# Kernel tuning notes

Measured on AMD Instinct MI355X. Metric: run time of the kernel, lower is better.

Reference implementation:

```python
import jax, jax.numpy as jnp
import numpy as np

B, L, D = 4, 2048, 1024
H = 16
HD = D // H


def setup_inputs() -> dict:
    key = jax.random.key(0)
    ks = jax.random.split(key, 6)
    x = jax.random.normal(ks[0], (B, L, D), dtype=jnp.float32)
    # True = masked-out (strict upper triangle -> causal)
    causal_mask = jnp.triu(jnp.ones((L, L), dtype=bool), k=1)
    key_padding_mask = jnp.zeros((B, L), dtype=bool)  # no padding
    lim = 1.0 / np.sqrt(D)
    Wqkv = jax.random.uniform(ks[1], (3 * D, D), minval=-lim, maxval=lim, dtype=jnp.float32)
    bqkv = jax.random.uniform(ks[2], (3 * D,), minval=-lim, maxval=lim, dtype=jnp.float32)
    Wproj = jax.random.uniform(ks[3], (D, D), minval=-lim, maxval=lim, dtype=jnp.float32)
    bproj = jax.random.uniform(ks[4], (D,), minval=-lim, maxval=lim, dtype=jnp.float32)
    return {"x": x, "causal_mask": causal_mask, "key_padding_mask": key_padding_mask,
            "Wqkv": Wqkv, "bqkv": bqkv, "Wproj": Wproj, "bproj": bproj}


def reference(x, causal_mask, key_padding_mask, Wqkv, bqkv, Wproj, bproj):
    b, l, d = x.shape
    scale = (d // H // 1) ** 0  # placeholder; real scale below
    scale = (d // H) ** -0.5
    qkv = x @ Wqkv.T + bqkv                      # [B,L,3D]
    qkv = qkv.reshape(b, l, 3, H, HD).transpose(2, 0, 3, 1, 4)  # [3,B,H,L,HD]
    q, k, v = qkv[0], qkv[1], qkv[2]
    attn = jnp.einsum('bhqd,bhkd->bhqk', q, k) * scale          # [B,H,L,L]
    neg_inf = jnp.float32(-jnp.inf)
    attn = jnp.where(causal_mask[None, None, :, :], neg_inf, attn)
    attn = jnp.where(key_padding_mask[:, None, None, :], neg_inf, attn)
    attn = jax.nn.softmax(attn, axis=-1)
    attn = jnp.nan_to_num(attn, nan=0.0, posinf=0.0, neginf=0.0)
    out = jnp.einsum('bhqk,bhkd->bhqd', attn, v)                # [B,H,L,HD]
    out = out.transpose(0, 2, 1, 3).reshape(b, l, d)
    return out @ Wproj.T + bproj
```

## Files before the change

### kernel.cpp

```cpp
#include <hip/hip_runtime.h>

typedef __bf16 bf16;
typedef __attribute__((ext_vector_type(8))) __bf16 bf16x8;
typedef __attribute__((ext_vector_type(4))) __bf16 bf16x4;
typedef __attribute__((ext_vector_type(4))) float f32x4;
typedef __attribute__((ext_vector_type(4))) short short4v;

#define AS1C(p) ((const __attribute__((address_space(1))) void*)(p))
#define AS3(p)  ((__attribute__((address_space(3))) void*)(p))

static __device__ __forceinline__ f32x4 pv_mfma(bf16x4 a, bf16x4 b, f32x4 c) {
#if __has_builtin(__builtin_amdgcn_mfma_f32_16x16x16bf16_1k)
  return __builtin_amdgcn_mfma_f32_16x16x16bf16_1k(
      __builtin_bit_cast(short4v, a), __builtin_bit_cast(short4v, b), c, 0, 0, 0);
#else
  f32x4 d = c;
  asm("v_mfma_f32_16x16x16_bf16 %0, %1, %2, %0" : "+v"(d) : "v"(a), "v"(b));
  return d;
#endif
}

__global__ void castk(const float* __restrict__ in, bf16* __restrict__ out, long n) {
  long i = ((long)blockIdx.x * blockDim.x + threadIdx.x) * 4;
  if (i >= n) return;
  f32x4 v = *reinterpret_cast<const f32x4*>(in + i);
  bf16x4 o;
  o[0] = (bf16)v[0]; o[1] = (bf16)v[1]; o[2] = (bf16)v[2]; o[3] = (bf16)v[3];
  *reinterpret_cast<bf16x4*>(out + i) = o;
}

template<int MODE>
__global__ __launch_bounds__(256, 2)
void gemm_bt(const bf16* __restrict__ A, const bf16* __restrict__ BT,
             const float* __restrict__ bias, void* __restrict__ Cout,
             int M, int N, int K) {
  __shared__ bf16 As[128 * 64];
  __shared__ bf16 Bs[128 * 64];
  const int tid = threadIdx.x;
  const int lane = tid & 63;
  const int w = tid >> 6;
  const int wm = w >> 1, wn = w & 1;
  const int row0 = blockIdx.y * 128, col0 = blockIdx.x * 128;

  f32x4 acc[4][4] = {};

  const int srow = tid >> 3;
  const int scb = ((tid & 7) << 4) ^ ((srow & 7) << 4);
  const long aoff = (long)(row0 + srow) * K + (scb >> 1);
  const long boff = (long)(col0 + srow) * K + (scb >> 1);

  for (int k0 = 0; k0 < K; k0 += 64) {
    #pragma unroll
    for (int i = 0; i < 4; ++i) {
      __builtin_amdgcn_global_load_lds(AS1C(A + aoff + (long)i * 32 * K + k0),
                                       AS3((char*)As + i * 4096 + w * 1024), 16, 0, 0);
      __builtin_amdgcn_global_load_lds(AS1C(BT + boff + (long)i * 32 * K + k0),
                                       AS3((char*)Bs + i * 4096 + w * 1024), 16, 0, 0);
    }
    __syncthreads();
    #pragma unroll
    for (int kf = 0; kf < 2; ++kf) {
      bf16x8 af[4], bfr[4];
      #pragma unroll
      for (int m = 0; m < 4; ++m) {
        int r = wm * 64 + m * 16 + (lane & 15);
        int cb = (kf * 64 + ((lane >> 4) << 4)) ^ ((r & 7) << 4);
        af[m] = *reinterpret_cast<const bf16x8*>((const char*)As + r * 128 + cb);
      }
      #pragma unroll
      for (int n = 0; n < 4; ++n) {
        int r = wn * 64 + n * 16 + (lane & 15);
        int cb = (kf * 64 + ((lane >> 4) << 4)) ^ ((r & 7) << 4);
        bfr[n] = *reinterpret_cast<const bf16x8*>((const char*)Bs + r * 128 + cb);
      }
      #pragma unroll
      for (int m = 0; m < 4; ++m)
        #pragma unroll
        for (int n = 0; n < 4; ++n) {
          if constexpr (MODE == 1)
            acc[m][n] = __builtin_amdgcn_mfma_f32_16x16x32_bf16(bfr[n], af[m], acc[m][n], 0, 0, 0);
          else
            acc[m][n] = __builtin_amdgcn_mfma_f32_16x16x32_bf16(af[m], bfr[n], acc[m][n], 0, 0, 0);
        }
    }
    __syncthreads();
  }

  const int g = lane >> 4, q = lane & 15;

  if constexpr (MODE == 0) {
    #pragma unroll
    for (int m = 0; m < 4; ++m)
      #pragma unroll
      for (int n = 0; n < 4; ++n)
        #pragma unroll
        for (int r = 0; r < 4; ++r) {
          int grow = row0 + wm * 64 + m * 16 + g * 4 + r;
          int gcol = col0 + wn * 64 + n * 16 + q;
          reinterpret_cast<float*>(Cout)[(long)grow * N + gcol] = acc[m][n][r] + bias[gcol];
        }
  } else if constexpr (MODE == 1) {
    const int t = (int)blockIdx.x >> 3;
    const int h = (((int)blockIdx.x << 1) | wn) & 15;
    const float qs = (t == 0) ? 0.125f : 1.0f;
    bf16* outb = reinterpret_cast<bf16*>(Cout) + (t ? 8388608 : 0);
    #pragma unroll
    for (int n = 0; n < 4; ++n) {
      f32x4 bv = *reinterpret_cast<const f32x4*>(bias + col0 + wn * 64 + n * 16 + g * 4);
      #pragma unroll
      for (int m = 0; m < 4; ++m) {
        int grow = row0 + wm * 64 + m * 16 + q;
        int bb = grow >> 11, ll = grow & 2047;
        bf16x4 o;
        #pragma unroll
        for (int r = 0; r < 4; ++r) o[r] = (bf16)((acc[m][n][r] + bv[r]) * qs);
        *reinterpret_cast<bf16x4*>(outb + ((long)(bb * 16 + h) * 2048 + ll) * 64 + n * 16 + g * 4) = o;
      }
    }
  } else {
    const int h = (((int)blockIdx.x << 1) | wn) & 15;
    bf16* outb = reinterpret_cast<bf16*>(Cout);
    #pragma unroll
    for (int n = 0; n < 4; ++n) {
      float bv = bias[col0 + wn * 64 + n * 16 + q];
      int hd = n * 16 + q;
      #pragma unroll
      for (int m = 0; m < 4; ++m) {
        int grow = row0 + wm * 64 + m * 16 + g * 4;
        int bb = grow >> 11, ll = grow & 2047;
        bf16x4 o;
        #pragma unroll
        for (int r = 0; r < 4; ++r) o[r] = (bf16)(acc[m][n][r] + bv);
        *reinterpret_cast<bf16x4*>(outb + ((long)(bb * 16 + h) * 64 + hd) * 2048 + ll) = o;
      }
    }
  }
}

__global__ __launch_bounds__(256, 4)
void attn_fwd(const bf16* __restrict__ Qg, const bf16* __restrict__ Kg,
              const bf16* __restrict__ VTg, bf16* __restrict__ Og) {
  __shared__ bf16 Ks[2][64 * 64];
  __shared__ bf16 Vs[2][64 * 64];
  const int tid = threadIdx.x, lane = tid & 63, w = tid >> 6;
  const int g = lane >> 4, q = lane & 15;

  const int orig = blockIdx.x;
  const int wgid = (orig & 7) * 256 + (orig >> 3);
  const int bh = wgid >> 5;
  const int qi = 31 - (wgid & 31);
  const int bb = bh >> 4, h = bh & 15;
  const long base = (long)bh * (2048 * 64);
  const int qw = qi * 64 + w * 16;
  const int myq = qw + q;

  bf16x8 qf[2];
  qf[0] = *reinterpret_cast<const bf16x8*>(Qg + base + (long)myq * 64 + g * 8);
  qf[1] = *reinterpret_cast<const bf16x8*>(Qg + base + (long)myq * 64 + 32 + g * 8);

  f32x4 accO[4] = {};
  float m = -1e30f, l = 0.f;

  const int srow = tid >> 3;
  const int scb = ((tid & 7) << 4) ^ ((srow & 7) << 4);
  const int nt = qi + 1;

  auto stage = [&](int kt, int buf) {
    #pragma unroll
    for (int i = 0; i < 2; ++i) {
      __builtin_amdgcn_global_load_lds(
          AS1C(Kg + base + (long)(kt * 64 + i * 32 + srow) * 64 + (scb >> 1)),
          AS3((char*)&Ks[buf][0] + i * 4096 + w * 1024), 16, 0, 0);
      __builtin_amdgcn_global_load_lds(
          AS1C(VTg + base + (long)(i * 32 + srow) * 2048 + kt * 64 + (scb >> 1)),
          AS3((char*)&Vs[buf][0] + i * 4096 + w * 1024), 16, 0, 0);
    }
  };

  stage(0, 0);

  for (int kt = 0; kt < nt; ++kt) {
    const int cur = kt & 1;
    __syncthreads();
    if (kt + 1 < nt) stage(kt + 1, cur ^ 1);

    const char* Kb = (const char*)&Ks[cur][0];
    const char* Vb = (const char*)&Vs[cur][0];

    f32x4 sT[4] = {};
    #pragma unroll
    for (int kf = 0; kf < 2; ++kf) {
      #pragma unroll
      for (int a = 0; a < 4; ++a) {
        int r = a * 16 + q;
        int cb = (kf * 64 + g * 16) ^ ((r & 7) << 4);
        bf16x8 kb = *reinterpret_cast<const bf16x8*>(Kb + r * 128 + cb);
        sT[a] = __builtin_amdgcn_mfma_f32_16x16x32_bf16(kb, qf[kf], sT[a], 0, 0, 0);
      }
    }

    if (kt == qi) {
      #pragma unroll
      for (int a = 0; a < 4; ++a)
        #pragma unroll
        for (int r = 0; r < 4; ++r) {
          int kv = kt * 64 + a * 16 + 4 * g + r;
          if (kv > myq) sT[a][r] = -1e30f;
        }
    }

    float vm = -1e30f;
    #pragma unroll
    for (int a = 0; a < 4; ++a)
      #pragma unroll
      for (int r = 0; r < 4; ++r) vm = fmaxf(vm, sT[a][r]);
    vm = fmaxf(vm, __shfl_xor(vm, 16));
    vm = fmaxf(vm, __shfl_xor(vm, 32));
    float mnew = fmaxf(m, vm);
    float fac = __expf(m - mnew);
    m = mnew;

    float ps = 0.f;
    bf16x4 pa[4];
    #pragma unroll
    for (int a = 0; a < 4; ++a)
      #pragma unroll
      for (int r = 0; r < 4; ++r) {
        float p = __expf(sT[a][r] - mnew);
        ps += p;
        pa[a][r] = (bf16)p;
      }
    ps += __shfl_xor(ps, 16);
    ps += __shfl_xor(ps, 32);
    l = l * fac + ps;
    #pragma unroll
    for (int b = 0; b < 4; ++b) accO[b] *= fac;

    #pragma unroll
    for (int a = 0; a < 4; ++a) {
      #pragma unroll
      for (int b = 0; b < 4; ++b) {
        int row = b * 16 + q;
        int cb = (a * 32 + g * 8) ^ ((row & 7) << 4);
        bf16x4 vfrag = *reinterpret_cast<const bf16x4*>(Vb + row * 128 + cb);
        accO[b] = pv_mfma(vfrag, pa[a], accO[b]);
      }
    }
  }

  __syncthreads();
  char* ob = (char*)&Ks[0][0] + w * 2048;
  float rl = 1.0f / l;
  #pragma unroll
  for (int b = 0; b < 4; ++b)
    #pragma unroll
    for (int r = 0; r < 4; ++r) {
      int hd = 16 * b + 4 * g + r;
      int cb = (hd * 2) ^ ((q & 7) << 4);
      *reinterpret_cast<bf16*>(ob + q * 128 + cb) = (bf16)(accO[b][r] * rl);
    }
  asm volatile("s_waitcnt lgkmcnt(0)" ::: "memory");
  __builtin_amdgcn_sched_barrier(0);

  const int rr = lane >> 2, cc = lane & 3;
  #pragma unroll
  for (int half = 0; half < 2; ++half) {
    int hd0 = cc * 16 + half * 8;
    int cb = (hd0 * 2) ^ ((rr & 7) << 4);
    bf16x8 vv = *reinterpret_cast<const bf16x8*>(ob + rr * 128 + cb);
    *reinterpret_cast<bf16x8*>(Og + (long)(bb * 2048 + qw + rr) * 1024 + h * 64 + hd0) = vv;
  }
}

extern "C" void kernel_launch(void* const* d_in, const int* in_sizes, int n_in,
                              void* d_out, int out_size, void* d_ws, size_t ws_size,
                              hipStream_t stream) {
  (void)in_sizes; (void)n_in; (void)out_size; (void)ws_size;
  const float* x     = (const float*)d_in[0];
  const float* Wqkv  = (const float*)d_in[3];
  const float* bqkv  = (const float*)d_in[4];
  const float* Wproj = (const float*)d_in[5];
  const float* bproj = (const float*)d_in[6];

  bf16* xb     = (bf16*)d_ws;
  bf16* Wqkvb  = xb + 8388608;
  bf16* Wprojb = Wqkvb + 3145728;
  bf16* Qb     = Wprojb + 1048576;
  bf16* Ob     = Qb + 3 * 8388608;

  castk<<<8192, 256, 0, stream>>>(x, xb, 8388608);
  castk<<<3072, 256, 0, stream>>>(Wqkv, Wqkvb, 3145728);
  castk<<<1024, 256, 0, stream>>>(Wproj, Wprojb, 1048576);

  gemm_bt<1><<<dim3(16, 64), 256, 0, stream>>>(xb, Wqkvb, bqkv, (void*)Qb, 8192, 3072, 1024);
  gemm_bt<2><<<dim3(8, 64), 256, 0, stream>>>(xb, Wqkvb + (long)2048 * 1024, bqkv + 2048,
                                              (void*)(Qb + 16777216), 8192, 3072, 1024);

  attn_fwd<<<dim3(2048), 256, 0, stream>>>(Qb, Qb + 8388608, Qb + 16777216, Ob);

  gemm_bt<0><<<dim3(8, 64), 256, 0, stream>>>(Ob, Wprojb, bproj, d_out, 8192, 1024, 1024);
}
```

Before: 196.4 us.

## Enlarge GEMM tiles to 256x256 with double-buffered LDS and use exp2 softmax

Replaces the 128x128 single-buffered GEMM with a 512-thread 256x256 tile kernel. It double-buffers LDS so the next K-slice loads while the current one computes, aiming for more reuse per byte fetched and fewer barriers. Attention now folds log2(e) into the Q scale and uses the hardware exp2 instead of expf, and the max reduction uses three-input max trees. The larger tiles use 128KB of LDS and many accumulator registers, and they launch far fewer blocks (256, 128, 128), which may underfill the GPU's compute units.

```diff
diff --git a/kernel.cpp b/kernel.cpp
--- a/kernel.cpp
+++ b/kernel.cpp
@@ -20,6 +20,17 @@
 #endif
 }
 
+static __device__ __forceinline__ float fexp2(float x) {
+#if __has_builtin(__builtin_amdgcn_exp2f)
+  return __builtin_amdgcn_exp2f(x);
+#else
+  return exp2f(x);
+#endif
+}
+static __device__ __forceinline__ float m3(float a, float b, float c) {
+  return fmaxf(fmaxf(a, b), c);
+}
+
 __global__ void castk(const float* __restrict__ in, bf16* __restrict__ out, long n) {
   long i = ((long)blockIdx.x * blockDim.x + threadIdx.x) * 4;
   if (i >= n) return;
@@ -30,107 +41,115 @@
 }
 
 template<int MODE>
-__global__ __launch_bounds__(256, 2)
-void gemm_bt(const bf16* __restrict__ A, const bf16* __restrict__ BT,
-             const float* __restrict__ bias, void* __restrict__ Cout,
-             int M, int N, int K) {
-  __shared__ bf16 As[128 * 64];
-  __shared__ bf16 Bs[128 * 64];
+__global__ __launch_bounds__(512, 2)
+void gemm8(const bf16* __restrict__ A, const bf16* __restrict__ BT,
+           const float* __restrict__ bias, void* __restrict__ Cout,
+           int N, int K) {
+  __shared__ bf16 As[2][256 * 64];
+  __shared__ bf16 Bs[2][256 * 64];
   const int tid = threadIdx.x;
   const int lane = tid & 63;
   const int w = tid >> 6;
-  const int wm = w >> 1, wn = w & 1;
-  const int row0 = blockIdx.y * 128, col0 = blockIdx.x * 128;
-
-  f32x4 acc[4][4] = {};
-
-  const int srow = tid >> 3;
-  const int scb = ((tid & 7) << 4) ^ ((srow & 7) << 4);
-  const long aoff = (long)(row0 + srow) * K + (scb >> 1);
-  const long boff = (long)(col0 + srow) * K + (scb >> 1);
-
-  for (int k0 = 0; k0 < K; k0 += 64) {
-    #pragma unroll
-    for (int i = 0; i < 4; ++i) {
-      __builtin_amdgcn_global_load_lds(AS1C(A + aoff + (long)i * 32 * K + k0),
-                                       AS3((char*)As + i * 4096 + w * 1024), 16, 0, 0);
-      __builtin_amdgcn_global_load_lds(AS1C(BT + boff + (long)i * 32 * K + k0),
-                                       AS3((char*)Bs + i * 4096 + w * 1024), 16, 0, 0);
-    }
+  const int wm = w >> 2, wn = w & 3;
+  const int g = lane >> 4, q = lane & 15;
+  const int row0 = blockIdx.y * 256, col0 = blockIdx.x * 256;
+
+  f32x4 acc[8][4] = {};
+
+  const int sr = tid >> 3;
+  const int scb = ((tid & 7) << 4) ^ ((sr & 7) << 4);
+
+  auto stage = [&](int k0, int buf) {
+    #pragma unroll
+    for (int i = 0; i < 4; ++i)
+      __builtin_amdgcn_global_load_lds(
+          AS1C(A + (long)(row0 + i * 64 + sr) * K + k0 + (scb >> 1)),
+          AS3((char*)&As[buf][0] + i * 8192 + tid * 16), 16, 0, 0);
+    #pragma unroll
+    for (int i = 0; i < 4; ++i)
+      __builtin_amdgcn_global_load_lds(
+          AS1C(BT + (long)(col0 + i * 64 + sr) * K + k0 + (scb >> 1)),
+          AS3((char*)&Bs[buf][0] + i * 8192 + tid * 16), 16, 0, 0);
+  };
+
+  stage(0, 0);
+  const int NK = K >> 6;
+  for (int t = 0; t < NK; ++t) {
+    const int cur = t & 1;
     __syncthreads();
-    #pragma unroll
-    for (int kf = 0; kf < 2; ++kf) {
-      bf16x8 af[4], bfr[4];
-      #pragma unroll
-      for (int m = 0; m < 4; ++m) {
-        int r = wm * 64 + m * 16 + (lane & 15);
-        int cb = (kf * 64 + ((lane >> 4) << 4)) ^ ((r & 7) << 4);
-        af[m] = *reinterpret_cast<const bf16x8*>((const char*)As + r * 128 + cb);
-      }
-      #pragma unroll
-      for (int n = 0; n < 4; ++n) {
-        int r = wn * 64 + n * 16 + (lane & 15);
-        int cb = (kf * 64 + ((lane >> 4) << 4)) ^ ((r & 7) << 4);
-        bfr[n] = *reinterpret_cast<const bf16x8*>((const char*)Bs + r * 128 + cb);
-      }
-      #pragma unroll
-      for (int m = 0; m < 4; ++m)
-        #pragma unroll
-        for (int n = 0; n < 4; ++n) {
+    if (t + 1 < NK) stage((t + 1) << 6, cur ^ 1);
+    const char* Ab = (const char*)&As[cur][0];
+    const char* Bb = (const char*)&Bs[cur][0];
+    #pragma unroll
+    for (int kk = 0; kk < 2; ++kk) {
+      bf16x8 bfrag[4];
+      #pragma unroll
+      for (int ni = 0; ni < 4; ++ni) {
+        int rr = wn * 64 + ni * 16 + q;
+        int cb = (kk * 64 + g * 16) ^ ((rr & 7) << 4);
+        bfrag[ni] = *reinterpret_cast<const bf16x8*>(Bb + rr * 128 + cb);
+      }
+      #pragma unroll
+      for (int mi = 0; mi < 8; ++mi) {
+        int rr = wm * 128 + mi * 16 + q;
+        int cb = (kk * 64 + g * 16) ^ ((rr & 7) << 4);
+        bf16x8 afrag = *reinterpret_cast<const bf16x8*>(Ab + rr * 128 + cb);
+        #pragma unroll
+        for (int ni = 0; ni < 4; ++ni) {
           if constexpr (MODE == 1)
-            acc[m][n] = __builtin_amdgcn_mfma_f32_16x16x32_bf16(bfr[n], af[m], acc[m][n], 0, 0, 0);
+            acc[mi][ni] = __builtin_amdgcn_mfma_f32_16x16x32_bf16(bfrag[ni], afrag, acc[mi][ni], 0, 0, 0);
           else
-            acc[m][n] = __builtin_amdgcn_mfma_f32_16x16x32_bf16(af[m], bfr[n], acc[m][n], 0, 0, 0);
+            acc[mi][ni] = __builtin_amdgcn_mfma_f32_16x16x32_bf16(afrag, bfrag[ni], acc[mi][ni], 0, 0, 0);
         }
-    }
-    __syncthreads();
+      }
+    }
   }
 
-  const int g = lane >> 4, q = lane & 15;
-
   if constexpr (MODE == 0) {
     #pragma unroll
-    for (int m = 0; m < 4; ++m)
-      #pragma unroll
-      for (int n = 0; n < 4; ++n)
+    for (int mi = 0; mi < 8; ++mi)
+      #pragma unroll
+      for (int ni = 0; ni < 4; ++ni) {
+        int gcol = col0 + wn * 64 + ni * 16 + q;
+        float bv = bias[gcol];
         #pragma unroll
         for (int r = 0; r < 4; ++r) {
-          int grow = row0 + wm * 64 + m * 16 + g * 4 + r;
-          int gcol = col0 + wn * 64 + n * 16 + q;
-          reinterpret_cast<float*>(Cout)[(long)grow * N + gcol] = acc[m][n][r] + bias[gcol];
+          int grow = row0 + wm * 128 + mi * 16 + g * 4 + r;
+          reinterpret_cast<float*>(Cout)[(long)grow * N + gcol] = acc[mi][ni][r] + bv;
         }
+      }
   } else if constexpr (MODE == 1) {
-    const int t = (int)blockIdx.x >> 3;
-    const int h = (((int)blockIdx.x << 1) | wn) & 15;
-    const float qs = (t == 0) ? 0.125f : 1.0f;
-    bf16* outb = reinterpret_cast<bf16*>(Cout) + (t ? 8388608 : 0);
-    #pragma unroll
-    for (int n = 0; n < 4; ++n) {
-      f32x4 bv = *reinterpret_cast<const f32x4*>(bias + col0 + wn * 64 + n * 16 + g * 4);
-      #pragma unroll
-      for (int m = 0; m < 4; ++m) {
-        int grow = row0 + wm * 64 + m * 16 + q;
+    const int tt = (int)blockIdx.x >> 2;
+    const int h = ((int)blockIdx.x * 4 + wn) & 15;
+    const float qs = (tt == 0) ? 0.125f * 1.44269504f : 1.0f;
+    bf16* outb = reinterpret_cast<bf16*>(Cout) + (tt ? 8388608 : 0);
+    #pragma unroll
+    for (int ni = 0; ni < 4; ++ni) {
+      f32x4 bv = *reinterpret_cast<const f32x4*>(bias + col0 + wn * 64 + ni * 16 + g * 4);
+      #pragma unroll
+      for (int mi = 0; mi < 8; ++mi) {
+        int grow = row0 + wm * 128 + mi * 16 + q;
         int bb = grow >> 11, ll = grow & 2047;
         bf16x4 o;
         #pragma unroll
-        for (int r = 0; r < 4; ++r) o[r] = (bf16)((acc[m][n][r] + bv[r]) * qs);
-        *reinterpret_cast<bf16x4*>(outb + ((long)(bb * 16 + h) * 2048 + ll) * 64 + n * 16 + g * 4) = o;
+        for (int r = 0; r < 4; ++r) o[r] = (bf16)((acc[mi][ni][r] + bv[r]) * qs);
+        *reinterpret_cast<bf16x4*>(outb + ((long)(bb * 16 + h) * 2048 + ll) * 64 + ni * 16 + g * 4) = o;
       }
     }
   } else {
-    const int h = (((int)blockIdx.x << 1) | wn) & 15;
+    const int h = ((int)blockIdx.x * 4 + wn) & 15;
     bf16* outb = reinterpret_cast<bf16*>(Cout);
     #pragma unroll
-    for (int n = 0; n < 4; ++n) {
-      float bv = bias[col0 + wn * 64 + n * 16 + q];
-      int hd = n * 16 + q;
-      #pragma unroll
-      for (int m = 0; m < 4; ++m) {
-        int grow = row0 + wm * 64 + m * 16 + g * 4;
+    for (int ni = 0; ni < 4; ++ni) {
+      float bv = bias[col0 + wn * 64 + ni * 16 + q];
+      int hd = ni * 16 + q;
+      #pragma unroll
+      for (int mi = 0; mi < 8; ++mi) {
+        int grow = row0 + wm * 128 + mi * 16 + g * 4;
         int bb = grow >> 11, ll = grow & 2047;
         bf16x4 o;
         #pragma unroll
-        for (int r = 0; r < 4; ++r) o[r] = (bf16)(acc[m][n][r] + bv);
+        for (int r = 0; r < 4; ++r) o[r] = (bf16)(acc[mi][ni][r] + bv);
         *reinterpret_cast<bf16x4*>(outb + ((long)(bb * 16 + h) * 64 + hd) * 2048 + ll) = o;
       }
     }
@@ -148,10 +167,10 @@
   const int orig = blockIdx.x;
   const int wgid = (orig & 7) * 256 + (orig >> 3);
   const int bh = wgid >> 5;
-  const int qi = 31 - (wgid & 31);
+  const int qt = 31 - (wgid & 31);
   const int bb = bh >> 4, h = bh & 15;
   const long base = (long)bh * (2048 * 64);
-  const int qw = qi * 64 + w * 16;
+  const int qw = qt * 64 + w * 16;
   const int myq = qw + q;
 
   bf16x8 qf[2];
@@ -163,7 +182,7 @@
 
   const int srow = tid >> 3;
   const int scb = ((tid & 7) << 4) ^ ((srow & 7) << 4);
-  const int nt = qi + 1;
+  const int nt = qt + 1;
 
   auto stage = [&](int kt, int buf) {
     #pragma unroll
@@ -199,7 +218,7 @@
       }
     }
 
-    if (kt == qi) {
+    if (kt == qt) {
       #pragma unroll
       for (int a = 0; a < 4; ++a)
         #pragma unroll
@@ -209,15 +228,16 @@
         }
     }
 
-    float vm = -1e30f;
-    #pragma unroll
-    for (int a = 0; a < 4; ++a)
-      #pragma unroll
-      for (int r = 0; r < 4; ++r) vm = fmaxf(vm, sT[a][r]);
+    float t0 = m3(sT[0][0], sT[0][1], sT[0][2]);
+    float t1 = m3(sT[0][3], sT[1][0], sT[1][1]);
+    float t2 = m3(sT[1][2], sT[1][3], sT[2][0]);
+    float t3 = m3(sT[2][1], sT[2][2], sT[2][3]);
+    float t4 = m3(sT[3][0], sT[3][1], sT[3][2]);
+    float vm = fmaxf(m3(t0, t1, t2), m3(t3, t4, sT[3][3]));
     vm = fmaxf(vm, __shfl_xor(vm, 16));
     vm = fmaxf(vm, __shfl_xor(vm, 32));
     float mnew = fmaxf(m, vm);
-    float fac = __expf(m - mnew);
+    float fac = fexp2(m - mnew);
     m = mnew;
 
     float ps = 0.f;
@@ -226,7 +246,7 @@
     for (int a = 0; a < 4; ++a)
       #pragma unroll
       for (int r = 0; r < 4; ++r) {
-        float p = __expf(sT[a][r] - mnew);
+        float p = fexp2(sT[a][r] - mnew);
         ps += p;
         pa[a][r] = (bf16)p;
       }
@@ -292,11 +312,11 @@
   castk<<<3072, 256, 0, stream>>>(Wqkv, Wqkvb, 3145728);
   castk<<<1024, 256, 0, stream>>>(Wproj, Wprojb, 1048576);
 
-  gemm_bt<1><<<dim3(16, 64), 256, 0, stream>>>(xb, Wqkvb, bqkv, (void*)Qb, 8192, 3072, 1024);
-  gemm_bt<2><<<dim3(8, 64), 256, 0, stream>>>(xb, Wqkvb + (long)2048 * 1024, bqkv + 2048,
-                                              (void*)(Qb + 16777216), 8192, 3072, 1024);
+  gemm8<1><<<dim3(8, 32), 512, 0, stream>>>(xb, Wqkvb, bqkv, (void*)Qb, 2048, 1024);
+  gemm8<2><<<dim3(4, 32), 512, 0, stream>>>(xb, Wqkvb + (long)2048 * 1024, bqkv + 2048,
+                                            (void*)(Qb + 16777216), 1024, 1024);
 
   attn_fwd<<<dim3(2048), 256, 0, stream>>>(Qb, Qb + 8388608, Qb + 16777216, Ob);
 
-  gemm_bt<0><<<dim3(8, 64), 256, 0, stream>>>(Ob, Wprojb, bproj, d_out, 8192, 1024, 1024);
-}
+  gemm8<0><<<dim3(4, 32), 512, 0, stream>>>(Ob, Wprojb, bproj, d_out, 1024, 1024);
+}
```

Result: slower. 228.0 us, median of 5 (+16.1%).
